# Optimization experiments

Measured on AMD Instinct MI355X. Metric: run time of the kernel, lower is better.

The kernel has to match this reference:

```python
import jax, jax.numpy as jnp
import numpy as np

T, B, D, BF = 512, 256, 256, 2  # time (nodes/tree), batch, feature dim, branching factor


def setup_inputs() -> dict:
    key = jax.random.key(0)
    k1, k2, k3 = jax.random.split(key, 3)
    inputs = jax.random.normal(k1, (T, B, D), dtype=jnp.float32)
    # Valid postfix (shift-reduce) arity sequence: two leaves, then alternate
    # combine(2)/leaf(0) -> left-comb binary tree; keeps stack pointer in range.
    t = np.arange(T)
    ar = np.where((t >= 2) & (t % 2 == 0), 2, 0).astype(np.int64)
    arities = jnp.asarray(np.broadcast_to(ar[:, None], (T, B)))
    scale = 1.0 / np.sqrt(D)
    W_in = jax.random.normal(k2, (D, D), dtype=jnp.float32) * scale
    W_ch = jax.random.normal(k3, (BF, D, D), dtype=jnp.float32) * scale
    b = jnp.zeros((D,), dtype=jnp.float32)
    return {"inputs": inputs, "arities": arities, "W_in": W_in, "W_ch": W_ch, "b": b}


def reference(inputs, arities, W_in, W_ch, b):
    Tn, Bn, Dn = inputs.shape
    bf = W_ch.shape[0]
    k = jnp.arange(Bn)

    def unit(x, children):
        # tree-RNN cell: tanh(x@W_in + sum_i child_i@W_ch[i] + b)
        h = x @ W_in + b
        for i in range(bf):
            h = h + children[i] @ W_ch[i]
        return jnp.tanh(h)

    memory0 = jnp.zeros((Tn, Bn, Dn), dtype=inputs.dtype)
    stack0 = jnp.zeros((Bn, Tn + bf), dtype=arities.dtype)
    ptr0 = jnp.full((Bn,), bf - 1, dtype=arities.dtype)

    def step(carry, xs):
        memory, stack, ptr = carry
        x_t, ar, t = xs
        children = []
        for i in range(bf):
            idx = stack[k, ptr - i]                    # [B] top-of-stack pointers
            entry = memory[idx, k]                     # [B, D] gather child features
            mask = (ar > i).astype(entry.dtype)[:, None]
            children.append(entry * mask)              # zero absent children
        new_entry = unit(x_t, children)
        memory = memory.at[t].set(new_entry)           # scatter to memory slot t
        ptr = ptr - jnp.abs(ar) + 1                    # pop arity, push 1
        ignore = ar == -1
        # stack[k,ptr] *= ignore; += t*(1-ignore)  <=>  keep old if ignore else t
        stack = stack.at[k, ptr].set(jnp.where(ignore, stack[k, ptr], t))
        return (memory, stack, ptr), None

    (memory, stack, ptr), _ = jax.lax.scan(
        step, (memory0, stack0, ptr0), (inputs, arities, jnp.arange(Tn)))
    out = memory[stack[k, ptr], k]                     # [B, D] tree roots
    return (out, memory)
```

## Files before the change

### kernel.cpp

```cpp
#include <hip/hip_runtime.h>
#include <hip/hip_bf16.h>


constexpr int T = 512, B = 256, D = 256;

constexpr int WS_CNT  = 0;
constexpr int WS_ROOT = 16;
constexpr int WS_NW   = 272;
constexpr int WS_L0   = 1024;
constexpr int WS_L1   = WS_L0 + T * B;
constexpr int WS_WORK = WS_L1 + T * B;

__global__ __launch_bounds__(256) void k_stack(const int* __restrict__ ar,
                                               unsigned* __restrict__ ws) {
  __shared__ int ar_l[T];
  __shared__ int S[1024];
  __shared__ unsigned lbuf0[T];
  __shared__ unsigned lbuf1[T];
  __shared__ unsigned wbuf[1024];
  __shared__ int cnts[4];
  __shared__ unsigned base0, base1;

  int k = blockIdx.x;
  int tid = threadIdx.x;
  ar_l[tid]       = ar[tid * B + k];
  ar_l[tid + 256] = ar[(tid + 256) * B + k];
  S[tid] = 0; S[tid + 256] = 0; S[tid + 512] = 0; S[tid + 768] = 0;
  __syncthreads();

  if (tid == 0) {
    int ptr = 1;
    int top = 0, next = 0;
    int n0 = 0, n1 = 0, nw = 0;
    for (int t = 0; t < T; t++) {
      int a = ar_l[t];
      int aa = a < 0 ? -a : a;
      unsigned cc[2]; int ncc = 0;
      if (a > 0) {
        int c0 = top;
        if (ar_l[c0] <= 0)
          lbuf0[n0++] = (unsigned)c0 | ((unsigned)t << 9) | ((unsigned)k << 18);
        else
          cc[ncc++] = (unsigned)c0;
        if (a > 1) {
          int c1 = next;
          if (ar_l[c1] <= 0)
            lbuf1[n1++] = (unsigned)c1 | ((unsigned)t << 9) | ((unsigned)k << 18);
          else
            cc[ncc++] = (unsigned)c1 | (1u << 18);
        }
      }
      if (a >= 1) {
        if (ncc == 0) {
          wbuf[nw++] = (unsigned)t | (1u << 19) | (1u << 20);
        } else {
          for (int e = 0; e < ncc; e++) {
            unsigned w = (unsigned)t | ((cc[e] & 511u) << 9) |
                         (((cc[e] >> 18) & 1u) << 18) | (1u << 21);
            if (e == 0) w |= (1u << 19);
            if (e == ncc - 1) w |= (1u << 20);
            wbuf[nw++] = w;
          }
        }
      }
      int pnew = ptr - aa + 1;
      if (a != -1) {
        S[pnew & 1023] = t;
        if (aa == 0)      { next = top; top = t; }
        else if (aa == 1) { top = t; }
        else              { top = t; next = S[(pnew - 1) & 1023]; }
      }
      ptr = pnew;
    }
    cnts[0] = n0; cnts[1] = n1; cnts[2] = nw;
    cnts[3] = S[ptr & 1023];
    base0 = atomicAdd(ws + WS_CNT + 0, (unsigned)n0);
    base1 = atomicAdd(ws + WS_CNT + 1, (unsigned)n1);
  }
  __syncthreads();
  int n0 = cnts[0], n1 = cnts[1], nw = cnts[2];
  for (int i = tid; i < n0; i += 256) ws[WS_L0 + base0 + i] = lbuf0[i];
  for (int i = tid; i < n1; i += 256) ws[WS_L1 + base1 + i] = lbuf1[i];
  for (int i = tid; i < nw; i += 256) ws[WS_WORK + k * 1024 + i] = wbuf[i];
  if (tid == 0) { ws[WS_NW + k] = (unsigned)nw; ws[WS_ROOT + k] = (unsigned)cnts[3]; }
}

__global__ __launch_bounds__(256) void k_gemm_h(const float* __restrict__ X,
                                                const float* __restrict__ W,
                                                const float* __restrict__ bias,
                                                const int* __restrict__ ar,
                                                float* __restrict__ Hm) {
  int row0 = blockIdx.x * 64;
  __shared__ __align__(16) float As[16][68];
  __shared__ __align__(16) float Bs[16][256];
  __shared__ int lar[64];
  int tid = threadIdx.x;
  if (tid < 64) lar[tid] = ar[row0 + tid];
  int cq = tid & 31, rg = tid >> 5;
  float acc[8][8];
  float4 b_lo = *(const float4*)&bias[cq * 4];
  float4 b_hi = *(const float4*)&bias[128 + cq * 4];
#pragma unroll
  for (int rr = 0; rr < 8; rr++) {
    acc[rr][0] = b_lo.x; acc[rr][1] = b_lo.y; acc[rr][2] = b_lo.z; acc[rr][3] = b_lo.w;
    acc[rr][4] = b_hi.x; acc[rr][5] = b_hi.y; acc[rr][6] = b_hi.z; acc[rr][7] = b_hi.w;
  }
  int sr = tid >> 2;
  int skc = (tid & 3) * 4;
  for (int kk = 0; kk < 256; kk += 16) {
    float4 a4 = *(const float4*)&X[(row0 + sr) * 256 + kk + skc];
    As[skc + 0][sr] = a4.x; As[skc + 1][sr] = a4.y;
    As[skc + 2][sr] = a4.z; As[skc + 3][sr] = a4.w;
#pragma unroll
    for (int i = 0; i < 4; i++) {
      int idx = tid + i * 256;
      int r = idx >> 6, c4 = idx & 63;
      *(float4*)&Bs[r][c4 * 4] = *(const float4*)&W[(kk + r) * 256 + c4 * 4];
    }
    __syncthreads();
#pragma unroll
    for (int kc = 0; kc < 16; kc++) {
      float4 a0  = *(const float4*)&As[kc][rg * 8];
      float4 a1  = *(const float4*)&As[kc][rg * 8 + 4];
      float4 blo = *(const float4*)&Bs[kc][cq * 4];
      float4 bhi = *(const float4*)&Bs[kc][128 + cq * 4];
      float a[8]  = {a0.x, a0.y, a0.z, a0.w, a1.x, a1.y, a1.z, a1.w};
      float bb[8] = {blo.x, blo.y, blo.z, blo.w, bhi.x, bhi.y, bhi.z, bhi.w};
#pragma unroll
      for (int rr = 0; rr < 8; rr++)
#pragma unroll
        for (int q = 0; q < 8; q++) acc[rr][q] += a[rr] * bb[q];
    }
    __syncthreads();
  }
#pragma unroll
  for (int rr = 0; rr < 8; rr++) {
    int row = rg * 8 + rr;
    bool leaf = lar[row] <= 0;
    float4 lo, hi;
    lo.x = acc[rr][0]; lo.y = acc[rr][1]; lo.z = acc[rr][2]; lo.w = acc[rr][3];
    hi.x = acc[rr][4]; hi.y = acc[rr][5]; hi.z = acc[rr][6]; hi.w = acc[rr][7];
    if (leaf) {
      lo.x = tanhf(lo.x); lo.y = tanhf(lo.y); lo.z = tanhf(lo.z); lo.w = tanhf(lo.w);
      hi.x = tanhf(hi.x); hi.y = tanhf(hi.y); hi.z = tanhf(hi.z); hi.w = tanhf(hi.w);
    }
    float* dst = &Hm[(row0 + row) * 256];
    *(float4*)&dst[cq * 4] = lo;
    *(float4*)&dst[128 + cq * 4] = hi;
  }
}

__global__ __launch_bounds__(256) void k_leafgemm(const float* __restrict__ Hm,
                                                  float* __restrict__ Gm,
                                                  const float* __restrict__ Wch,
                                                  const unsigned* __restrict__ list,
                                                  const unsigned* __restrict__ cntp,
                                                  int which) {
  unsigned cnt = *cntp;
  unsigned tile0 = blockIdx.x * 64;
  if (tile0 >= cnt) return;
  int ne = (int)min(64u, cnt - tile0);
  __shared__ unsigned ent[64];
  __shared__ __align__(16) float As[16][68];
  __shared__ __align__(16) float Bs[16][256];
  int tid = threadIdx.x;
  if (tid < 64) ent[tid] = (tid < ne) ? list[tile0 + tid] : 0u;
  __syncthreads();
  const float* W = Wch + which * (D * D);
  int cq = tid & 31, rg = tid >> 5;
  float acc[8][8];
#pragma unroll
  for (int rr = 0; rr < 8; rr++)
#pragma unroll
    for (int q = 0; q < 8; q++) acc[rr][q] = 0.0f;
  int sr = tid >> 2;
  int skc = (tid & 3) * 4;
  unsigned se = ent[sr];
  int sc = (int)(se & 511u), skb = (int)((se >> 18) & 255u);
  const float* srow = &Hm[((sc << 8) + skb) * 256];
  for (int kk = 0; kk < 256; kk += 16) {
    float4 a4;
    if (sr < ne) a4 = *(const float4*)&srow[kk + skc];
    else { a4.x = a4.y = a4.z = a4.w = 0.0f; }
    As[skc + 0][sr] = a4.x; As[skc + 1][sr] = a4.y;
    As[skc + 2][sr] = a4.z; As[skc + 3][sr] = a4.w;
#pragma unroll
    for (int i = 0; i < 4; i++) {
      int idx = tid + i * 256;
      int r = idx >> 6, c4 = idx & 63;
      *(float4*)&Bs[r][c4 * 4] = *(const float4*)&W[(kk + r) * 256 + c4 * 4];
    }
    __syncthreads();
#pragma unroll
    for (int kc = 0; kc < 16; kc++) {
      float4 a0  = *(const float4*)&As[kc][rg * 8];
      float4 a1  = *(const float4*)&As[kc][rg * 8 + 4];
      float4 blo = *(const float4*)&Bs[kc][cq * 4];
      float4 bhi = *(const float4*)&Bs[kc][128 + cq * 4];
      float a[8]  = {a0.x, a0.y, a0.z, a0.w, a1.x, a1.y, a1.z, a1.w};
      float bb[8] = {blo.x, blo.y, blo.z, blo.w, bhi.x, bhi.y, bhi.z, bhi.w};
#pragma unroll
      for (int rr = 0; rr < 8; rr++)
#pragma unroll
        for (int q = 0; q < 8; q++) acc[rr][q] += a[rr] * bb[q];
    }
    __syncthreads();
  }
#pragma unroll
  for (int rr = 0; rr < 8; rr++) {
    int e = rg * 8 + rr;
    if (e < ne) {
      unsigned en = ent[e];
      int t = (int)((en >> 9) & 511u), kb = (int)((en >> 18) & 255u);
      float* dst = &Gm[((t << 8) + kb) * 256];
      float4 lo = *(const float4*)&dst[cq * 4];
      float4 hi = *(const float4*)&dst[128 + cq * 4];
      lo.x += acc[rr][0]; lo.y += acc[rr][1]; lo.z += acc[rr][2]; lo.w += acc[rr][3];
      hi.x += acc[rr][4]; hi.y += acc[rr][5]; hi.z += acc[rr][6]; hi.w += acc[rr][7];
      *(float4*)&dst[cq * 4] = lo;
      *(float4*)&dst[128 + cq * 4] = hi;
    }
  }
}

__global__ __launch_bounds__(512, 2) void k_seq(float* __restrict__ Mm,
                                                const float* __restrict__ Wch,
                                                const unsigned* __restrict__ ws) {
  int k = blockIdx.x;
  int tid = threadIdx.x;
  int j = tid & 255, h = tid >> 8;
  __shared__ __align__(16) float crow[256];
  __shared__ float partial[256];
  __shared__ int cached;
  if (tid == 0) cached = -1;
  float w[128];
  const float* W1 = Wch + D * D;
#pragma unroll
  for (int p = 0; p < 128; p++) w[p] = W1[(h * 128 + p) * 256 + j];
  int nw = (int)ws[WS_NW + k];
  const unsigned* work = ws + WS_WORK + k * 1024;
  float acc = 0.0f;
  __syncthreads();
  unsigned e = (nw > 0) ? work[0] : 0u;
  float nb = 0.0f;
  if (nw > 0 && ((e >> 19) & 1u) && h == 0)
    nb = Mm[(((int)(e & 511u) << 8) + k) * 256 + j];
  for (int n = 0; n < nw; n++) {
    unsigned cur = e;
    unsigned nxt = (n + 1 < nw) ? work[n + 1] : 0u;
    int t = (int)(cur & 511u), c = (int)((cur >> 9) & 511u);
    int wi = (int)((cur >> 18) & 1u);
    bool first = (cur >> 19) & 1u, last = (cur >> 20) & 1u, hasc = (cur >> 21) & 1u;
    if (first) acc = (h == 0) ? nb : 0.0f;
    float nb2 = 0.0f;
    if ((n + 1 < nw) && ((nxt >> 19) & 1u) && h == 0)
      nb2 = Mm[(((int)(nxt & 511u) << 8) + k) * 256 + j];
    if (hasc) {
      if (c != cached) {
        asm volatile("s_waitcnt vmcnt(0) lgkmcnt(0)" ::: "memory");
        __builtin_amdgcn_s_barrier();
        __builtin_amdgcn_sched_barrier(0);
        if (tid < 256) crow[tid] = Mm[((c << 8) + k) * 256 + tid];
        if (tid == 0) cached = c;
        asm volatile("s_waitcnt vmcnt(0) lgkmcnt(0)" ::: "memory");
        __builtin_amdgcn_s_barrier();
        __builtin_amdgcn_sched_barrier(0);
      }
      if (wi == 1) {
#pragma unroll
        for (int p = 0; p < 32; p++) {
          float4 c4 = ((const float4*)crow)[h * 32 + p];
          acc += c4.x * w[4 * p] + c4.y * w[4 * p + 1] +
                 c4.z * w[4 * p + 2] + c4.w * w[4 * p + 3];
        }
      } else {
        const float* W0 = Wch;
#pragma unroll 8
        for (int p = 0; p < 128; p++)
          acc += crow[h * 128 + p] * W0[(h * 128 + p) * 256 + j];
      }
    }
    if (last) {
      if (h == 1) partial[j] = acc;
      __builtin_amdgcn_sched_barrier(0);
      asm volatile("s_waitcnt lgkmcnt(0)" ::: "memory");
      __builtin_amdgcn_s_barrier();
      __builtin_amdgcn_sched_barrier(0);
      if (h == 0) {
        float v = tanhf(acc + partial[j]);
        Mm[((t << 8) + k) * 256 + j] = v;
        crow[j] = v;
      }
      if (tid == 0) cached = t;
      __builtin_amdgcn_sched_barrier(0);
      asm volatile("s_waitcnt lgkmcnt(0)" ::: "memory");
      __builtin_amdgcn_s_barrier();
      __builtin_amdgcn_sched_barrier(0);
    }
    e = nxt; nb = nb2;
  }
}

__global__ __launch_bounds__(256) void k_root(const float* __restrict__ Mm,
                                              float* __restrict__ out,
                                              const unsigned* __restrict__ ws) {
  int k = blockIdx.x;
  unsigned r = ws[WS_ROOT + k];
  out[k * 256 + threadIdx.x] = Mm[(((int)r << 8) + k) * 256 + threadIdx.x];
}

extern "C" void kernel_launch(void* const* d_in, const int* in_sizes, int n_in,
                              void* d_out, int out_size, void* d_ws, size_t ws_size,
                              hipStream_t stream) {
  const float* X    = (const float*)d_in[0];
  const int*   AR   = (const int*)d_in[1];
  const float* Win  = (const float*)d_in[2];
  const float* Wch  = (const float*)d_in[3];
  const float* bias = (const float*)d_in[4];
  float* out = (float*)d_out;
  float* Mm  = out + B * D;
  unsigned* ws = (unsigned*)d_ws;

  hipMemsetAsync(d_ws, 0, 512, stream);
  k_stack<<<B, 256, 0, stream>>>(AR, ws);
  k_gemm_h<<<(T * B) / 64, 256, 0, stream>>>(X, Win, bias, AR, Mm);
  k_leafgemm<<<(T * B) / 64, 256, 0, stream>>>(Mm, Mm, Wch, ws + WS_L0, ws + WS_CNT + 0, 0);
  k_leafgemm<<<(T * B) / 64, 256, 0, stream>>>(Mm, Mm, Wch, ws + WS_L1, ws + WS_CNT + 1, 1);
  k_seq<<<B, 512, 0, stream>>>(Mm, Wch, ws);
  k_root<<<B, 256, 0, stream>>>(Mm, out, ws);
}
```

Baseline: 1.041 ms.

## Repartition sequential tree-RNN matvec into 8-way K split with packed f2 FMAs

The sequential per-batch kernel changes its work split. Previously 512 threads each owned one output column and half of K. Now each thread owns four output columns over a 32-element K slice, giving 8 partial sums per column that are reduced through shared memory. Weights are held in registers as float2 pairs so the compiler can emit packed FMA instructions, and the child row buffer is double-buffered, which removes one shared-memory write hazard and keeps the cached index in a register. The cost is a larger 8-way reduction in shared memory on every node and vectorized loads from global memory in the W0 path.

```diff
diff --git a/kernel.cpp b/kernel.cpp
--- a/kernel.cpp
+++ b/kernel.cpp
@@ -3,6 +3,9 @@
 
 
 constexpr int T = 512, B = 256, D = 256;
+
+typedef float f2 __attribute__((ext_vector_type(2)));
+typedef float f4 __attribute__((ext_vector_type(4)));
 
 constexpr int WS_CNT  = 0;
 constexpr int WS_ROOT = 16;
@@ -228,74 +231,98 @@
                                                 const unsigned* __restrict__ ws) {
   int k = blockIdx.x;
   int tid = threadIdx.x;
-  int j = tid & 255, h = tid >> 8;
-  __shared__ __align__(16) float crow[256];
-  __shared__ float partial[256];
-  __shared__ int cached;
-  if (tid == 0) cached = -1;
-  float w[128];
+  int cs = tid & 63;
+  int ps = tid >> 6;
+  __shared__ __align__(16) float crow[2][256];
+  __shared__ __align__(16) float partial[8][256];
+  f2 w01[32], w23[32];
   const float* W1 = Wch + D * D;
 #pragma unroll
-  for (int p = 0; p < 128; p++) w[p] = W1[(h * 128 + p) * 256 + j];
+  for (int q = 0; q < 32; q++) {
+    f4 wv = *(const f4*)&W1[(32 * ps + q) * 256 + 4 * cs];
+    w01[q] = __builtin_shufflevector(wv, wv, 0, 1);
+    w23[q] = __builtin_shufflevector(wv, wv, 2, 3);
+  }
+#pragma unroll
+  for (int q = 0; q < 32; q++) {
+    asm volatile("" : "+v"(w01[q]));
+    asm volatile("" : "+v"(w23[q]));
+  }
   int nw = (int)ws[WS_NW + k];
   const unsigned* work = ws + WS_WORK + k * 1024;
-  float acc = 0.0f;
+  int cached = -1;
+  int rb = 0;
   __syncthreads();
   unsigned e = (nw > 0) ? work[0] : 0u;
   float nb = 0.0f;
-  if (nw > 0 && ((e >> 19) & 1u) && h == 0)
-    nb = Mm[(((int)(e & 511u) << 8) + k) * 256 + j];
+  if (nw > 0 && ((e >> 19) & 1u) && tid < 256)
+    nb = Mm[(((int)(e & 511u) << 8) + k) * 256 + tid];
+  f2 a01 = {0.0f, 0.0f}, a23 = {0.0f, 0.0f};
   for (int n = 0; n < nw; n++) {
     unsigned cur = e;
     unsigned nxt = (n + 1 < nw) ? work[n + 1] : 0u;
     int t = (int)(cur & 511u), c = (int)((cur >> 9) & 511u);
     int wi = (int)((cur >> 18) & 1u);
     bool first = (cur >> 19) & 1u, last = (cur >> 20) & 1u, hasc = (cur >> 21) & 1u;
-    if (first) acc = (h == 0) ? nb : 0.0f;
+    if (first) { a01 = (f2){0.0f, 0.0f}; a23 = (f2){0.0f, 0.0f}; }
     float nb2 = 0.0f;
-    if ((n + 1 < nw) && ((nxt >> 19) & 1u) && h == 0)
-      nb2 = Mm[(((int)(nxt & 511u) << 8) + k) * 256 + j];
+    if ((n + 1 < nw) && ((nxt >> 19) & 1u) && tid < 256)
+      nb2 = Mm[(((int)(nxt & 511u) << 8) + k) * 256 + tid];
     if (hasc) {
       if (c != cached) {
         asm volatile("s_waitcnt vmcnt(0) lgkmcnt(0)" ::: "memory");
         __builtin_amdgcn_s_barrier();
         __builtin_amdgcn_sched_barrier(0);
-        if (tid < 256) crow[tid] = Mm[((c << 8) + k) * 256 + tid];
-        if (tid == 0) cached = c;
+        if (tid < 256) crow[rb][tid] = Mm[((c << 8) + k) * 256 + tid];
+        cached = c;
         asm volatile("s_waitcnt vmcnt(0) lgkmcnt(0)" ::: "memory");
         __builtin_amdgcn_s_barrier();
         __builtin_amdgcn_sched_barrier(0);
       }
+      const f4* hb = (const f4*)&crow[rb][32 * ps];
       if (wi == 1) {
 #pragma unroll
-        for (int p = 0; p < 32; p++) {
-          float4 c4 = ((const float4*)crow)[h * 32 + p];
-          acc += c4.x * w[4 * p] + c4.y * w[4 * p + 1] +
-                 c4.z * w[4 * p + 2] + c4.w * w[4 * p + 3];
+        for (int q8 = 0; q8 < 8; q8++) {
+          f4 h4 = hb[q8];
+          f2 hx = {h4.x, h4.x}, hy = {h4.y, h4.y};
+          f2 hz = {h4.z, h4.z}, hw = {h4.w, h4.w};
+          a01 += hx * w01[4 * q8 + 0]; a23 += hx * w23[4 * q8 + 0];
+          a01 += hy * w01[4 * q8 + 1]; a23 += hy * w23[4 * q8 + 1];
+          a01 += hz * w01[4 * q8 + 2]; a23 += hz * w23[4 * q8 + 2];
+          a01 += hw * w01[4 * q8 + 3]; a23 += hw * w23[4 * q8 + 3];
         }
       } else {
         const float* W0 = Wch;
-#pragma unroll 8
-        for (int p = 0; p < 128; p++)
-          acc += crow[h * 128 + p] * W0[(h * 128 + p) * 256 + j];
+#pragma unroll 4
+        for (int q = 0; q < 32; q++) {
+          float hv = crow[rb][32 * ps + q];
+          f4 wv = *(const f4*)&W0[(32 * ps + q) * 256 + 4 * cs];
+          a01.x += hv * wv.x; a01.y += hv * wv.y;
+          a23.x += hv * wv.z; a23.y += hv * wv.w;
+        }
       }
     }
     if (last) {
-      if (h == 1) partial[j] = acc;
+      f4 pv = {a01.x, a01.y, a23.x, a23.y};
+      *(f4*)&partial[ps][4 * cs] = pv;
       __builtin_amdgcn_sched_barrier(0);
       asm volatile("s_waitcnt lgkmcnt(0)" ::: "memory");
       __builtin_amdgcn_s_barrier();
       __builtin_amdgcn_sched_barrier(0);
-      if (h == 0) {
-        float v = tanhf(acc + partial[j]);
-        Mm[((t << 8) + k) * 256 + j] = v;
-        crow[j] = v;
-      }
-      if (tid == 0) cached = t;
+      if (tid < 256) {
+        float s = nb;
+#pragma unroll
+        for (int m = 0; m < 8; m++) s += partial[m][tid];
+        float v = tanhf(s);
+        crow[rb ^ 1][tid] = v;
+        Mm[((t << 8) + k) * 256 + tid] = v;
+      }
       __builtin_amdgcn_sched_barrier(0);
       asm volatile("s_waitcnt lgkmcnt(0)" ::: "memory");
       __builtin_amdgcn_s_barrier();
       __builtin_amdgcn_sched_barrier(0);
+      rb ^= 1;
+      cached = t;
     }
     e = nxt; nb = nb2;
   }
```

After: 914.9 us. 1.14x faster.
